# Kernel optimization log

Measured on AMD Instinct MI355X. Metric: run time of the kernel, lower is better.

## Reference

```python
import jax, jax.numpy as jnp
import numpy as np

N_NODES = 50000
N_EDGES = 1600000
IN_FEATS = 256
OUT_FEATS = 128
NEG_SLOPE = 0.2


def setup_inputs() -> dict:
    key = jax.random.key(0)
    k1, k2, k3, k4, k5, k6 = jax.random.split(key, 6)
    gain = np.sqrt(2.0)  # calculate_gain('relu')
    w_std = gain * np.sqrt(2.0 / (IN_FEATS + OUT_FEATS))  # xavier normal
    a_std = gain * np.sqrt(2.0 / (1 + OUT_FEATS))
    return {
        "feat": jax.random.normal(k1, (N_NODES, IN_FEATS), dtype=jnp.float32),
        "W": jax.random.normal(k2, (OUT_FEATS, IN_FEATS), dtype=jnp.float32) * w_std,
        "attn_l": jax.random.normal(k3, (1, OUT_FEATS), dtype=jnp.float32) * a_std,
        "attn_r": jax.random.normal(k4, (1, OUT_FEATS), dtype=jnp.float32) * a_std,
        "src": jax.random.randint(k5, (N_EDGES,), 0, N_NODES, dtype=jnp.int32),
        "dst": jax.random.randint(k6, (N_EDGES,), 0, N_NODES, dtype=jnp.int32),
    }


def reference(feat, W, attn_l, attn_r, src, dst):
    # h = fc(feat): [N, D]
    h = jnp.einsum("ni,di->nd", feat, W)
    # per-node attention logits
    el = jnp.sum(h * attn_l, axis=-1)  # [N]
    er = jnp.sum(h * attn_r, axis=-1)  # [N]
    # apply_edge: e_uv = el[u] + er[v], then leaky relu
    e = jax.nn.leaky_relu(el[src] + er[dst], NEG_SLOPE)  # [E]
    # edge softmax over incoming edges of each destination node
    m = jax.ops.segment_max(e, dst, num_segments=N_NODES)  # [N]
    m = jnp.where(jnp.isneginf(m), 0.0, m)  # nodes with no in-edges
    ex = jnp.exp(e - m[dst])  # [E]
    denom = jax.ops.segment_sum(ex, dst, num_segments=N_NODES)  # [N]
    alpha = ex / jnp.maximum(denom[dst], 1e-9)  # [E]
    # gspmv: rst[v] = sum_{(u->v)} alpha_uv * h[u]
    rst = jax.ops.segment_sum(h[src] * alpha[:, None], dst, num_segments=N_NODES)
    return rst
```

## Files before the change

kernel.cpp:

```cpp
#include <hip/hip_runtime.h>
#include <hip/hip_bf16.h>


#define IN_FEATS 256
#define OUT_FEATS 128
#define NBINS 256
#define CAPB_LOG 14
#define CAPB (1 << CAPB_LOG)
#define SCAT_BLOCKS 512

typedef __bf16 bf16x8 __attribute__((ext_vector_type(8)));
typedef float f32x4 __attribute__((ext_vector_type(4)));

__global__ void prep(const float* __restrict__ W, __bf16* __restrict__ Wb, int nw,
                     int* __restrict__ cur) {
    int i = blockIdx.x * 256 + threadIdx.x;
    if (i < nw) Wb[i] = (__bf16)W[i];
    if (i < NBINS) cur[i] = i << CAPB_LOG;
}

__global__ __launch_bounds__(256) void gemm_scatter(
    const float* __restrict__ feat, const __bf16* __restrict__ Wb,
    const float* __restrict__ attn_l, const float* __restrict__ attn_r,
    __bf16* __restrict__ hb, float* __restrict__ el, float* __restrict__ er,
    const int* __restrict__ src, const int* __restrict__ dst,
    int* __restrict__ bin_cur, unsigned* __restrict__ arena,
    int n, int E, int G) {
    __shared__ int h[NBINS];
    __shared__ int base[NBINS];

    if (blockIdx.x >= G) {
        const int blk = blockIdx.x - G;
        const int t = threadIdx.x;
        h[t] = 0;
        __syncthreads();
        const int chunk = (E + SCAT_BLOCKS - 1) / SCAT_BLOCKS;
        const int beg = blk * chunk;
        const int end = min(beg + chunk, E);
        for (int i = beg + t; i < end; i += 256)
            atomicAdd(&h[dst[i] >> 8], 1);
        __syncthreads();
        if (h[t] > 0)
            base[t] = atomicAdd(&bin_cur[t], h[t]);
        h[t] = 0;
        __syncthreads();
        for (int i = beg + t; i < end; i += 256) {
            int d = dst[i];
            int bin = d >> 8;
            int pos = base[bin] + atomicAdd(&h[bin], 1);
            pos = min(pos, ((bin + 1) << CAPB_LOG) - 1);
            arena[pos] = ((unsigned)d << 16) | (unsigned)src[i];
        }
        return;
    }

    const int wid = threadIdx.x >> 6;
    const int lane = threadIdx.x & 63;
    const int s = lane & 15;
    const int q = lane >> 4;
    const int m0 = blockIdx.x * 64 + wid * 16;
    if (m0 >= n) return;

    const int mrow = min(m0 + s, n - 1);
    const float* arow = feat + (size_t)mrow * IN_FEATS + q * 8;

    f32x4 acc[8];
#pragma unroll
    for (int nt = 0; nt < 8; nt++) acc[nt] = (f32x4){0.f, 0.f, 0.f, 0.f};

#pragma unroll
    for (int ks = 0; ks < 8; ks++) {
        const int k0 = ks * 32;
        float4 f0 = *(const float4*)(arow + k0);
        float4 f1 = *(const float4*)(arow + k0 + 4);
        bf16x8 a;
        a[0] = (__bf16)f0.x; a[1] = (__bf16)f0.y; a[2] = (__bf16)f0.z; a[3] = (__bf16)f0.w;
        a[4] = (__bf16)f1.x; a[5] = (__bf16)f1.y; a[6] = (__bf16)f1.z; a[7] = (__bf16)f1.w;
#pragma unroll
        for (int nt = 0; nt < 8; nt++) {
            bf16x8 b = *(const bf16x8*)(Wb + (size_t)(nt * 16 + s) * IN_FEATS + k0 + q * 8);
            acc[nt] = __builtin_amdgcn_mfma_f32_16x16x32_bf16(a, b, acc[nt], 0, 0, 0);
        }
    }

    float al[8], ar[8];
#pragma unroll
    for (int nt = 0; nt < 8; nt++) {
        al[nt] = attn_l[nt * 16 + s];
        ar[nt] = attn_r[nt * 16 + s];
    }

#pragma unroll
    for (int r = 0; r < 4; r++) {
        const int row = m0 + q * 4 + r;
        const bool ok = row < n;
        float pl = 0.f, pr = 0.f;
#pragma unroll
        for (int nt = 0; nt < 8; nt++) {
            float v = acc[nt][r];
            if (ok) hb[(size_t)row * OUT_FEATS + nt * 16 + s] = (__bf16)v;
            pl += v * al[nt];
            pr += v * ar[nt];
        }
#pragma unroll
        for (int m = 1; m < 16; m <<= 1) {
            pl += __shfl_xor(pl, m);
            pr += __shfl_xor(pr, m);
        }
        if (ok && s == 0) {
            el[row] = pl;
            er[row] = pr;
        }
    }
}

__global__ __launch_bounds__(512) void build_csr(const unsigned* __restrict__ arena,
                                                 const int* __restrict__ bin_cur,
                                                 const float* __restrict__ el,
                                                 const float* __restrict__ er,
                                                 unsigned* __restrict__ edges,
                                                 int* __restrict__ row_beg,
                                                 int* __restrict__ row_end,
                                                 int N, int edges_cap) {
    __shared__ unsigned lds[CAPB];
    __shared__ int cnt[256];
    __shared__ int off[256];
    const int b = blockIdx.x;
    const int t = threadIdx.x;
    const int abeg = b << CAPB_LOG;
    const int cnt_in = min(bin_cur[b] - abeg, CAPB);

    for (int i = t; i < cnt_in; i += 512) lds[i] = arena[abeg + i];
    if (t < 256) cnt[t] = 0;
    __syncthreads();

    for (int i = t; i < cnt_in; i += 512)
        atomicAdd(&cnt[(lds[i] >> 16) & 255], 1);
    __syncthreads();
    if (t < 256) off[t] = cnt[t];
    __syncthreads();
    for (int o = 1; o < 256; o <<= 1) {
        int v = (t < 256 && t >= o) ? off[t - o] : 0;
        __syncthreads();
        if (t < 256) off[t] += v;
        __syncthreads();
    }
    int mycnt = 0, excl = 0;
    if (t < 256) {
        mycnt = cnt[t];
        excl = off[t] - mycnt;
    }
    __syncthreads();
    if (t < 256) {
        off[t] = excl;
        int v = (b << 8) + t;
        if (v < N) {
            row_beg[v] = abeg + excl;
            row_end[v] = abeg + excl + mycnt;
        }
        cnt[t] = 0;
    }
    __syncthreads();

    for (int i = t; i < cnt_in; i += 512) {
        unsigned e = lds[i];
        int d8 = (e >> 16) & 255;
        int u = (int)(e & 0xFFFFu);
        float x = el[u] + er[(b << 8) + d8];
        x = (x > 0.f) ? x : 0.2f * x;
        float w = __expf(x);
        int r = atomicAdd(&cnt[d8], 1);
        int pos = abeg + off[d8] + r;
        pos = min(pos, edges_cap - 1);
        edges[pos] = (__float_as_uint(w) & 0xFFFF0000u) | (unsigned)u;
    }
}

__global__ __launch_bounds__(256) void gat_kernel(const __bf16* __restrict__ hb,
                                                  const unsigned* __restrict__ edges,
                                                  const int* __restrict__ row_beg,
                                                  const int* __restrict__ row_end,
                                                  float* __restrict__ out, int n) {
    const int v = blockIdx.x * 4 + (threadIdx.x >> 6);
    if (v >= n) return;
    const int lane = threadIdx.x & 63;
    const int beg = row_beg[v];
    const int end = row_end[v];
    const unsigned* hbu = (const unsigned*)hb;

    float acc0 = 0.f, acc1 = 0.f, wsum = 0.f;
    for (int c0 = beg; c0 < end; c0 += 64) {
        const int nn = min(64, end - c0);
        int my = (c0 + lane < end) ? (int)edges[c0 + lane] : 0;

        int k = 0;
        for (; k + 8 <= nn; k += 8) {
#pragma unroll
            for (int tt = 0; tt < 8; tt++) {
                unsigned e = (unsigned)__shfl(my, k + tt);
                int u = (int)(e & 0xFFFFu);
                float w = __uint_as_float(e & 0xFFFF0000u);
                wsum += w;
                unsigned pair = hbu[(size_t)u * (OUT_FEATS / 2) + lane];
                acc0 += w * __uint_as_float(pair << 16);
                acc1 += w * __uint_as_float(pair & 0xffff0000u);
            }
        }
        for (; k < nn; k++) {
            unsigned e = (unsigned)__shfl(my, k);
            int u = (int)(e & 0xFFFFu);
            float w = __uint_as_float(e & 0xFFFF0000u);
            wsum += w;
            unsigned pair = hbu[(size_t)u * (OUT_FEATS / 2) + lane];
            acc0 += w * __uint_as_float(pair << 16);
            acc1 += w * __uint_as_float(pair & 0xffff0000u);
        }
    }
    const float dnm = fmaxf(wsum, 1e-9f);
    float2 o = make_float2(acc0 / dnm, acc1 / dnm);
    *(float2*)(out + (size_t)v * OUT_FEATS + lane * 2) = o;
}

extern "C" void kernel_launch(void* const* d_in, const int* in_sizes, int n_in,
                              void* d_out, int out_size, void* d_ws, size_t ws_size,
                              hipStream_t stream) {
    const float* feat   = (const float*)d_in[0];
    const float* W      = (const float*)d_in[1];
    const float* attn_l = (const float*)d_in[2];
    const float* attn_r = (const float*)d_in[3];
    const int*   src    = (const int*)d_in[4];
    const int*   dst    = (const int*)d_in[5];
    const int N = in_sizes[0] / IN_FEATS;
    const int E = in_sizes[4];
    float* out = (float*)d_out;

    char* p = (char*)d_ws;
    auto alloc = [&](size_t bytes) -> char* {
        char* r = p;
        p += (bytes + 255) & ~(size_t)255;
        return r;
    };
    const int nbuckets = (N + 255) / 256;
    const int edges_cap = nbuckets * CAPB;

    __bf16* hb    = (__bf16*)alloc((size_t)N * OUT_FEATS * sizeof(__bf16));
    __bf16* Wb    = (__bf16*)alloc((size_t)OUT_FEATS * IN_FEATS * sizeof(__bf16));
    float* el     = (float*)alloc((size_t)N * sizeof(float));
    float* er     = (float*)alloc((size_t)N * sizeof(float));
    int*   bin_cur = (int*)alloc((size_t)NBINS * sizeof(int));
    int*   row_beg = (int*)alloc((size_t)N * sizeof(int));
    int*   row_end = (int*)alloc((size_t)N * sizeof(int));
    unsigned* arena = (unsigned*)alloc((size_t)NBINS * CAPB * sizeof(unsigned));
    unsigned* edges = (unsigned*)alloc((size_t)edges_cap * sizeof(unsigned));

    prep<<<dim3((OUT_FEATS * IN_FEATS + 255) / 256), dim3(256), 0, stream>>>(
        W, Wb, OUT_FEATS * IN_FEATS, bin_cur);

    const int G = (N + 63) / 64;
    gemm_scatter<<<dim3(G + SCAT_BLOCKS), dim3(256), 0, stream>>>(
        feat, Wb, attn_l, attn_r, hb, el, er, src, dst, bin_cur, arena, N, E, G);

    build_csr<<<dim3(nbuckets), dim3(512), 0, stream>>>(arena, bin_cur, el, er, edges,
                                                        row_beg, row_end, N, edges_cap);

    gat_kernel<<<dim3((N + 3) / 4), dim3(256), 0, stream>>>(hb, edges, row_beg,
                                                            row_end, out, N);
}
```

Baseline: 207.7 us.

## Drop prep kernel, interleave scatter/GEMM blocks, vectorize edge loads, widen CSR blocks

Removes the W-to-bf16 prep kernel. The GEMM now converts fp32 W on the fly, and the bin cursor init becomes a memset of relative offsets. Scatter blocks are interleaved with GEMM blocks by odd/even block index, with one scatter block per GEMM block and int4-vectorized dst/src loads. build_csr moves to 1024 threads with vectorized uint4 arena loads. The changes aim to cut a launch, overlap the edge binning with the GEMM, and raise memory throughput, at the cost of redundant W conversion in every GEMM wave.

```diff
diff --git a/kernel.cpp b/kernel.cpp
--- a/kernel.cpp
+++ b/kernel.cpp
@@ -7,62 +7,82 @@
 #define NBINS 256
 #define CAPB_LOG 14
 #define CAPB (1 << CAPB_LOG)
-#define SCAT_BLOCKS 512
 
 typedef __bf16 bf16x8 __attribute__((ext_vector_type(8)));
 typedef float f32x4 __attribute__((ext_vector_type(4)));
 
-__global__ void prep(const float* __restrict__ W, __bf16* __restrict__ Wb, int nw,
-                     int* __restrict__ cur) {
-    int i = blockIdx.x * 256 + threadIdx.x;
-    if (i < nw) Wb[i] = (__bf16)W[i];
-    if (i < NBINS) cur[i] = i << CAPB_LOG;
-}
-
 __global__ __launch_bounds__(256) void gemm_scatter(
-    const float* __restrict__ feat, const __bf16* __restrict__ Wb,
+    const float* __restrict__ feat, const float* __restrict__ W,
     const float* __restrict__ attn_l, const float* __restrict__ attn_r,
     __bf16* __restrict__ hb, float* __restrict__ el, float* __restrict__ er,
     const int* __restrict__ src, const int* __restrict__ dst,
     int* __restrict__ bin_cur, unsigned* __restrict__ arena,
-    int n, int E, int G) {
+    int n, int E, int chunk) {
     __shared__ int h[NBINS];
     __shared__ int base[NBINS];
 
-    if (blockIdx.x >= G) {
-        const int blk = blockIdx.x - G;
+    if (blockIdx.x & 1) {
+        const int blk = blockIdx.x >> 1;
         const int t = threadIdx.x;
         h[t] = 0;
         __syncthreads();
-        const int chunk = (E + SCAT_BLOCKS - 1) / SCAT_BLOCKS;
         const int beg = blk * chunk;
         const int end = min(beg + chunk, E);
-        for (int i = beg + t; i < end; i += 256)
-            atomicAdd(&h[dst[i] >> 8], 1);
+        for (int i0 = beg + t * 4; i0 < end; i0 += 1024) {
+            if (i0 + 4 <= end) {
+                int4 d4 = *(const int4*)(dst + i0);
+                atomicAdd(&h[d4.x >> 8], 1);
+                atomicAdd(&h[d4.y >> 8], 1);
+                atomicAdd(&h[d4.z >> 8], 1);
+                atomicAdd(&h[d4.w >> 8], 1);
+            } else {
+                for (int i = i0; i < end; i++) atomicAdd(&h[dst[i] >> 8], 1);
+            }
+        }
         __syncthreads();
         if (h[t] > 0)
             base[t] = atomicAdd(&bin_cur[t], h[t]);
         h[t] = 0;
         __syncthreads();
-        for (int i = beg + t; i < end; i += 256) {
-            int d = dst[i];
-            int bin = d >> 8;
-            int pos = base[bin] + atomicAdd(&h[bin], 1);
-            pos = min(pos, ((bin + 1) << CAPB_LOG) - 1);
-            arena[pos] = ((unsigned)d << 16) | (unsigned)src[i];
+        for (int i0 = beg + t * 4; i0 < end; i0 += 1024) {
+            if (i0 + 4 <= end) {
+                int4 d4 = *(const int4*)(dst + i0);
+                int4 s4 = *(const int4*)(src + i0);
+                int dd[4] = {d4.x, d4.y, d4.z, d4.w};
+                int ss[4] = {s4.x, s4.y, s4.z, s4.w};
+#pragma unroll
+                for (int k = 0; k < 4; k++) {
+                    int bin = dd[k] >> 8;
+                    int rel = base[bin] + atomicAdd(&h[bin], 1);
+                    rel = min(rel, CAPB - 1);
+                    arena[(bin << CAPB_LOG) + rel] =
+                        ((unsigned)dd[k] << 16) | (unsigned)ss[k];
+                }
+            } else {
+                for (int i = i0; i < end; i++) {
+                    int d = dst[i];
+                    int bin = d >> 8;
+                    int rel = base[bin] + atomicAdd(&h[bin], 1);
+                    rel = min(rel, CAPB - 1);
+                    arena[(bin << CAPB_LOG) + rel] =
+                        ((unsigned)d << 16) | (unsigned)src[i];
+                }
+            }
         }
         return;
     }
 
+    const int gblk = blockIdx.x >> 1;
     const int wid = threadIdx.x >> 6;
     const int lane = threadIdx.x & 63;
     const int s = lane & 15;
     const int q = lane >> 4;
-    const int m0 = blockIdx.x * 64 + wid * 16;
+    const int m0 = gblk * 64 + wid * 16;
     if (m0 >= n) return;
 
     const int mrow = min(m0 + s, n - 1);
     const float* arow = feat + (size_t)mrow * IN_FEATS + q * 8;
+    const float* wrow = W + (size_t)s * IN_FEATS + q * 8;
 
     f32x4 acc[8];
 #pragma unroll
@@ -78,7 +98,12 @@
         a[4] = (__bf16)f1.x; a[5] = (__bf16)f1.y; a[6] = (__bf16)f1.z; a[7] = (__bf16)f1.w;
 #pragma unroll
         for (int nt = 0; nt < 8; nt++) {
-            bf16x8 b = *(const bf16x8*)(Wb + (size_t)(nt * 16 + s) * IN_FEATS + k0 + q * 8);
+            const float* wp = wrow + (size_t)nt * 16 * IN_FEATS + k0;
+            float4 g0 = *(const float4*)wp;
+            float4 g1 = *(const float4*)(wp + 4);
+            bf16x8 b;
+            b[0] = (__bf16)g0.x; b[1] = (__bf16)g0.y; b[2] = (__bf16)g0.z; b[3] = (__bf16)g0.w;
+            b[4] = (__bf16)g1.x; b[5] = (__bf16)g1.y; b[6] = (__bf16)g1.z; b[7] = (__bf16)g1.w;
             acc[nt] = __builtin_amdgcn_mfma_f32_16x16x32_bf16(a, b, acc[nt], 0, 0, 0);
         }
     }
@@ -114,27 +139,32 @@
     }
 }
 
-__global__ __launch_bounds__(512) void build_csr(const unsigned* __restrict__ arena,
-                                                 const int* __restrict__ bin_cur,
-                                                 const float* __restrict__ el,
-                                                 const float* __restrict__ er,
-                                                 unsigned* __restrict__ edges,
-                                                 int* __restrict__ row_beg,
-                                                 int* __restrict__ row_end,
-                                                 int N, int edges_cap) {
+__global__ __launch_bounds__(1024) void build_csr(const unsigned* __restrict__ arena,
+                                                  const int* __restrict__ bin_cur,
+                                                  const float* __restrict__ el,
+                                                  const float* __restrict__ er,
+                                                  unsigned* __restrict__ edges,
+                                                  int* __restrict__ row_beg,
+                                                  int* __restrict__ row_end,
+                                                  int N, int edges_cap) {
     __shared__ unsigned lds[CAPB];
     __shared__ int cnt[256];
     __shared__ int off[256];
     const int b = blockIdx.x;
     const int t = threadIdx.x;
     const int abeg = b << CAPB_LOG;
-    const int cnt_in = min(bin_cur[b] - abeg, CAPB);
-
-    for (int i = t; i < cnt_in; i += 512) lds[i] = arena[abeg + i];
+    const int cnt_in = min(bin_cur[b], CAPB);
+
+    for (int i0 = t * 4; i0 < cnt_in; i0 += 4096) {
+        if (i0 + 4 <= cnt_in)
+            *(uint4*)&lds[i0] = *(const uint4*)(arena + abeg + i0);
+        else
+            for (int i = i0; i < cnt_in; i++) lds[i] = arena[abeg + i];
+    }
     if (t < 256) cnt[t] = 0;
     __syncthreads();
 
-    for (int i = t; i < cnt_in; i += 512)
+    for (int i = t; i < cnt_in; i += 1024)
         atomicAdd(&cnt[(lds[i] >> 16) & 255], 1);
     __syncthreads();
     if (t < 256) off[t] = cnt[t];
@@ -162,7 +192,7 @@
     }
     __syncthreads();
 
-    for (int i = t; i < cnt_in; i += 512) {
+    for (int i = t; i < cnt_in; i += 1024) {
         unsigned e = lds[i];
         int d8 = (e >> 16) & 255;
         int u = (int)(e & 0xFFFFu);
@@ -244,7 +274,6 @@
     const int edges_cap = nbuckets * CAPB;
 
     __bf16* hb    = (__bf16*)alloc((size_t)N * OUT_FEATS * sizeof(__bf16));
-    __bf16* Wb    = (__bf16*)alloc((size_t)OUT_FEATS * IN_FEATS * sizeof(__bf16));
     float* el     = (float*)alloc((size_t)N * sizeof(float));
     float* er     = (float*)alloc((size_t)N * sizeof(float));
     int*   bin_cur = (int*)alloc((size_t)NBINS * sizeof(int));
@@ -253,15 +282,16 @@
     unsigned* arena = (unsigned*)alloc((size_t)NBINS * CAPB * sizeof(unsigned));
     unsigned* edges = (unsigned*)alloc((size_t)edges_cap * sizeof(unsigned));
 
-    prep<<<dim3((OUT_FEATS * IN_FEATS + 255) / 256), dim3(256), 0, stream>>>(
-        W, Wb, OUT_FEATS * IN_FEATS, bin_cur);
+    hipMemsetAsync(bin_cur, 0, NBINS * sizeof(int), stream);
 
     const int G = (N + 63) / 64;
-    gemm_scatter<<<dim3(G + SCAT_BLOCKS), dim3(256), 0, stream>>>(
-        feat, Wb, attn_l, attn_r, hb, el, er, src, dst, bin_cur, arena, N, E, G);
-
-    build_csr<<<dim3(nbuckets), dim3(512), 0, stream>>>(arena, bin_cur, el, er, edges,
-                                                        row_beg, row_end, N, edges_cap);
+    const int chunk = (((E + G - 1) / G) + 3) & ~3;
+    gemm_scatter<<<dim3(2 * G), dim3(256), 0, stream>>>(
+        feat, W, attn_l, attn_r, hb, el, er, src, dst, bin_cur, arena, N, E, chunk);
+
+    build_csr<<<dim3(nbuckets), dim3(1024), 0, stream>>>(arena, bin_cur, el, er,
+                                                         edges, row_beg, row_end,
+                                                         N, edges_cap);
 
     gat_kernel<<<dim3((N + 3) / 4), dim3(256), 0, stream>>>(hb, edges, row_beg,
                                                             row_end, out, N);
```

Result: slower. 272.7 us (+31.3%).
